# Kernel optimization log

Measured on AMD Instinct MI355X. Metric: run time of the kernel, lower is better.

## Reference

```python
import jax, jax.numpy as jnp
import numpy as np
import math

N = 10000; E = 160000; B = 16
H = 256; TD = 128; NB = 4; NL = 3; NAT = 100; CD = 3


def _silu(x):
    return x * jax.nn.sigmoid(x)


def _mlp2(x, w1, b1, w2, b2):
    return _silu(x @ w1 + b1) @ w2 + b2


def _ln(x, g, b):
    m = jnp.mean(x, -1, keepdims=True)
    v = jnp.mean((x - m) ** 2, -1, keepdims=True)
    return (x - m) / jnp.sqrt(v + 1e-5) * g + b


def _fwd(x_atoms, pos, edge_index, batch_idx, timesteps, conditions, emb,
         te_w1, te_b1, te_w2, te_b2, ce_w1, ce_b1, ce_w2, ce_b2,
         tp_w1, tp_b1, tp_w2, tp_b2, nm_w1, nm_b1, nm_w2, nm_b2,
         em_w1, em_b1, em_w2, em_b2, ln_g, ln_b,
         ao_w1, ao_b1, ao_w2, ao_b2, co_w1, co_b1, co_w2, co_b2):
    n = x_atoms.shape[0]
    row, col = edge_index[0], edge_index[1]  # row = source (x_j), col = target (x_i)
    h = emb[x_atoms]  # [N, H]
    half = TD // 2
    freqs = jnp.exp(jnp.arange(half, dtype=jnp.float32) * (-math.log(10000.0) / (half - 1)))
    ang = timesteps.astype(jnp.float32)[:, None] * freqs[None, :]
    time_emb = _mlp2(jnp.concatenate([jnp.sin(ang), jnp.cos(ang)], -1), te_w1, te_b1, te_w2, te_b2)
    time_emb = time_emb + _mlp2(conditions, ce_w1, ce_b1, ce_w2, ce_b2)  # [B, TD]
    rel = pos[row] - pos[col]
    dist = jnp.sqrt(jnp.sum(rel * rel, -1, keepdims=True))  # [E, 1]
    counts = jnp.maximum(
        jax.ops.segment_sum(jnp.ones((row.shape[0],), jnp.float32), col, num_segments=n), 1.0)[:, None]
    for b in range(NB):
        h = h + _mlp2(time_emb, tp_w1[b], tp_b1[b], tp_w2[b], tp_b2[b])[batch_idx]
        for l in range(NL):
            # message: edge_mlp(concat(x_i, x_j, dist)); PyG x_i = target = col, x_j = source = row
            msg = _mlp2(jnp.concatenate([h[col], h[row], dist], -1),
                        em_w1[b, l], em_b1[b, l], em_w2[b, l], em_b2[b, l])  # [E, H]
            agg = jax.ops.segment_sum(msg, col, num_segments=n) / counts  # mean aggregation
            h_new = _mlp2(h, nm_w1[b, l], nm_b1[b, l], nm_w2[b, l], nm_b2[b, l]) + agg
            h = _ln(h + h_new, ln_g[b, l], ln_b[b, l])
    atom = _mlp2(h, ao_w1, ao_b1, ao_w2, ao_b2)  # [N, NAT]
    coord = _mlp2(h, co_w1, co_b1, co_w2, co_b2)  # [N, 3]
    return atom, coord


def setup_inputs() -> dict:
    key = jax.random.key(0)
    ks = jax.random.split(key, 48)
    ki = iter(ks)

    def nrm(shape, s=0.02):
        return jax.random.normal(next(ki), shape, jnp.float32) * s

    x_atoms = jax.random.randint(next(ki), (N,), 0, NAT)
    pos = jax.random.normal(next(ki), (N, 3), jnp.float32)
    row = jax.random.randint(next(ki), (E,), 0, N)
    off = jax.random.randint(next(ki), (E,), 1, N)
    col = (row + off) % N  # avoid self-loops so dist > 0
    edge_index = jnp.stack([row, col])
    batch_idx = jnp.sort(jax.random.randint(next(ki), (N,), 0, B))
    timesteps = jax.random.randint(next(ki), (B,), 0, 1000)
    conditions = jax.random.normal(next(ki), (B, CD), jnp.float32)
    z = lambda s: jnp.zeros(s, jnp.float32)
    params = dict(
        emb=nrm((NAT, H)),
        te_w1=nrm((TD, 2 * TD)), te_b1=z((2 * TD,)), te_w2=nrm((2 * TD, TD)), te_b2=z((TD,)),
        ce_w1=nrm((CD, H)), ce_b1=z((H,)), ce_w2=nrm((H, TD)), ce_b2=z((TD,)),
        tp_w1=nrm((NB, TD, H)), tp_b1=z((NB, H)), tp_w2=nrm((NB, H, H)), tp_b2=z((NB, H)),
        nm_w1=nrm((NB, NL, H, H)), nm_b1=z((NB, NL, H)), nm_w2=nrm((NB, NL, H, H)), nm_b2=z((NB, NL, H)),
        em_w1=nrm((NB, NL, 2 * H + 1, H)), em_b1=z((NB, NL, H)), em_w2=nrm((NB, NL, H, H)), em_b2=z((NB, NL, H)),
        ln_g=jnp.ones((NB, NL, H), jnp.float32), ln_b=z((NB, NL, H)),
        ao_w1=nrm((H, H)), ao_b1=z((H,)), ao_w2=nrm((H, NAT)), ao_b2=z((NAT,)),
        co_w1=nrm((H, H)), co_b1=z((H,)), co_w2=nrm((H, 3)), co_b2=z((3,)),
    )
    return dict(x_atoms=x_atoms, pos=pos, edge_index=edge_index, batch_idx=batch_idx,
                timesteps=timesteps, conditions=conditions, **params)


def reference(x_atoms, pos, edge_index, batch_idx, timesteps, conditions, emb,
              te_w1, te_b1, te_w2, te_b2, ce_w1, ce_b1, ce_w2, ce_b2,
              tp_w1, tp_b1, tp_w2, tp_b2, nm_w1, nm_b1, nm_w2, nm_b2,
              em_w1, em_b1, em_w2, em_b2, ln_g, ln_b,
              ao_w1, ao_b1, ao_w2, ao_b2, co_w1, co_b1, co_w2, co_b2):
    return _fwd(x_atoms, pos, edge_index, batch_idx, timesteps, conditions, emb,
                te_w1, te_b1, te_w2, te_b2, ce_w1, ce_b1, ce_w2, ce_b2,
                tp_w1, tp_b1, tp_w2, tp_b2, nm_w1, nm_b1, nm_w2, nm_b2,
                em_w1, em_b1, em_w2, em_b2, ln_g, ln_b,
                ao_w1, ao_b1, ao_w2, ao_b2, co_w1, co_b1, co_w2, co_b2)
```

## Files before the change

### kernel.cpp

```cpp
#include <hip/hip_runtime.h>

typedef unsigned short u16;
typedef __attribute__((ext_vector_type(8))) short   bf16x8;
typedef __attribute__((ext_vector_type(4))) float   f32x4;
typedef __attribute__((ext_vector_type(4))) unsigned short u16x4;
typedef __attribute__((ext_vector_type(2))) unsigned short u16x2;

#define DEV __device__ __forceinline__

DEV float bf2f(u16 u){ return __uint_as_float(((unsigned)u)<<16); }
DEV u16 f2bf(float f){ unsigned x=__float_as_uint(f); unsigned r=x+0x7fffu+((x>>16)&1u); return (u16)(r>>16); }
DEV float silu_f(float x){
  float e = __expf(-x);
  return x * __builtin_amdgcn_rcpf(1.f + e);
}
DEV float ldf(const void* p, long i, int isbf){
  float r;
  if (isbf) r = bf2f(((const u16*)p)[i]);
  else      r = ((const float*)p)[i];
  return r;
}
template<int ISBF> DEV float LD(const void* p, long i){
  if (ISBF) return bf2f(((const u16*)p)[i]);
  return ((const float*)p)[i];
}
DEV int detect_bf(const void* lng){
  return (((const unsigned*)lng)[0] == 0x3F800000u) ? 0 : 1;
}

#define GLDS(g,l) __builtin_amdgcn_global_load_lds((const __attribute__((address_space(1))) void*)(g), (__attribute__((address_space(3))) void*)(l), 16, 0, 0)

DEV int xcd_swz(int bid, int nwg){
  int q = nwg >> 3, r = nwg & 7;
  int x = bid & 7, l = bid >> 3;
  return (x < r ? x*(q+1) : r*(q+1) + (x-r)*q) + l;
}

struct WTJob {
  const void* in; u16* out;
  int inoff, ims, obase, oms, istride, Ncin, ors, gx, gy;
};
struct WTJobs { WTJob j[8]; int tile0[8]; };

template<int ISBF>
DEV void wtall_body(const WTJobs& J, int bidx, float* tile ){
  int ji = 0;
  #pragma unroll
  for (int j=1;j<8;j++) if (bidx >= J.tile0[j]) ji = j;
  const WTJob& job = J.j[ji];
  int ti = bidx - J.tile0[ji];
  int kx = ti % job.gx;
  int jy = (ti / job.gx) % job.gy;
  long m  = ti / (job.gx * job.gy);
  int k0 = kx*64, j0 = jy*64;
  int t = threadIdx.x;
  int c = t & 63, r4 = t >> 6;
  #pragma unroll
  for (int pass=0; pass<16; pass++){
    int k = k0 + pass*4 + r4;
    int j = j0 + c;
    float v = 0.f;
    if (j < job.Ncin) v = LD<ISBF>(job.in, (long)job.inoff + m*job.ims + (long)k*job.istride + j);
    tile[(pass*4 + r4)*65 + c] = v;
  }
  __syncthreads();
  #pragma unroll
  for (int pass=0; pass<16; pass++){
    int j = j0 + pass*4 + r4;
    int k = k0 + c;
    job.out[m*job.oms + job.obase + (long)j*job.ors + k] = f2bf(tile[c*65 + pass*4 + r4]);
  }
}

DEV void pack_body(int pb, int isbf,
    const void* nm_b1, const void* em_b1, const void* nm_b2, const void* em_b2,
    const void* ln_g, const void* ln_b, const void* em_w1,
    const void* ao_b1, const void* co_b1, const void* ao_b2,
    const void* co_w2, const void* co_b2, float* pp){
  int i = pb*256 + threadIdx.x;
  if (i >= 22887) return;
  const int T1 = 3072;
  float v;
  if      (i < T1)    v = ldf(nm_b1, i, isbf);
  else if (i < 2*T1)  v = ldf(em_b1, i-T1, isbf);
  else if (i < 3*T1)  v = ldf(nm_b2, i-2*T1, isbf);
  else if (i < 4*T1)  v = ldf(em_b2, i-3*T1, isbf);
  else if (i < 5*T1)  v = ldf(ln_g, i-4*T1, isbf);
  else if (i < 6*T1)  v = ldf(ln_b, i-5*T1, isbf);
  else if (i < 7*T1){ int j=i-6*T1; int li=j>>8; v = ldf(em_w1, (long)li*513*256 + 512*256 + (j&255), isbf); }
  else if (i < 22016){ int j=i-21504; v = (j<256) ? ldf(ao_b1,j,isbf) : ldf(co_b1,j-256,isbf); }
  else if (i < 22116) v = ldf(ao_b2, i-22016, isbf);
  else if (i < 22884) v = ldf(co_w2, i-22116, isbf);
  else                v = ldf(co_b2, i-22884, isbf);
  pp[i] = v;
}

template<int ISBF>
DEV void edgegeo_body(int eb, const int* ei, const void* pos, float* dist, int* cnt, int E){
  int e = eb*256 + threadIdx.x;
  if (e >= E) return;
  int r = ei[e], c = ei[E + e];
  float dx = LD<ISBF>(pos,(long)r*3+0) - LD<ISBF>(pos,(long)c*3+0);
  float dy = LD<ISBF>(pos,(long)r*3+1) - LD<ISBF>(pos,(long)c*3+1);
  float dz = LD<ISBF>(pos,(long)r*3+2) - LD<ISBF>(pos,(long)c*3+2);
  dist[e] = sqrtf(dx*dx + dy*dy + dz*dz);
  atomicAdd(&cnt[c], 1);
}

DEV void time_body_f32(const int* tsteps, const float* cond,
    const float* te_w1,const float* te_b1,const float* te_w2,const float* te_b2,
    const float* ce_w1,const float* ce_b1,const float* ce_w2,const float* ce_b2,
    const float* tp_w1,const float* tp_b1,const float* tp_w2,const float* tp_b2,
    float* tpe, float* smem){
  float* wbuf = smem;
  float* sa = smem + 16384;
  float* sb = sa + 256;
  float* tm = sb + 256;
  float* tb = tm + 256;
  const int b4 = blockIdx.x >> 4, b = blockIdx.x & 15, t = threadIdx.x;
  const int wbase = (t >> 6) * 256;

  auto TISSUE = [&](const float* src, int buf){
    float* d = wbuf + buf*8192 + wbase;
    #pragma unroll
    for (int r=0;r<8;r++)
      GLDS(src + (long)r*1024 + t*4, d + r*1024);
  };

  float ts = (float)tsteps[b];
  if (t < 64){
    float coef = (float)(-9.210340371976184/63.0);
    float fr = __expf(coef * (float)t);
    float ang = ts * fr;
    sa[t] = sinf(ang); sa[64+t] = cosf(ang);
  }
  TISSUE(te_w1, 0);
  __syncthreads();
  float a1 = te_b1[t];
  for (int c=0;c<4;c++){
    if (c<3) TISSUE(te_w1 + (c+1)*8192, (c+1)&1);
    const float* wb = wbuf + (c&1)*8192;
    #pragma unroll 8
    for (int k=0;k<32;k++) a1 = fmaf(sa[c*32+k], wb[k*256+t], a1);
    __syncthreads();
  }
  sb[t] = silu_f(a1);
  TISSUE(te_w2, 0);
  __syncthreads();
  float te = (t<128) ? te_b2[t] : 0.f;
  for (int c=0;c<4;c++){
    if (c<3) TISSUE(te_w2 + (c+1)*8192, (c+1)&1);
    const float* wb = wbuf + (c&1)*8192;
    if (t < 128){
      #pragma unroll 8
      for (int k=0;k<64;k++) te = fmaf(sb[c*64+k], wb[k*128+t], te);
    }
    __syncthreads();
  }
  {
    float a2 = ce_b1[t];
    #pragma unroll
    for (int k=0;k<3;k++) a2 = fmaf(cond[b*3+k], ce_w1[k*256+t], a2);
    sa[t] = silu_f(a2);
  }
  TISSUE(ce_w2, 0);
  __syncthreads();
  float ce = (t<128) ? ce_b2[t] : 0.f;
  for (int c=0;c<4;c++){
    if (c<3) TISSUE(ce_w2 + (c+1)*8192, (c+1)&1);
    const float* wb = wbuf + (c&1)*8192;
    if (t < 128){
      #pragma unroll 8
      for (int k=0;k<64;k++) ce = fmaf(sa[c*64+k], wb[k*128+t], ce);
    }
    __syncthreads();
  }
  if (t < 128) tb[t] = te + ce;
  const float* W5 = tp_w1 + (long)b4*128*256;
  TISSUE(W5, 0);
  __syncthreads();
  float a3 = tp_b1[b4*256 + t];
  for (int c=0;c<4;c++){
    if (c<3) TISSUE(W5 + (c+1)*8192, (c+1)&1);
    const float* wb = wbuf + (c&1)*8192;
    #pragma unroll 8
    for (int k=0;k<32;k++) a3 = fmaf(tb[c*32+k], wb[k*256+t], a3);
    __syncthreads();
  }
  tm[t] = silu_f(a3);
  const float* W6 = tp_w2 + (long)b4*256*256;
  TISSUE(W6, 0);
  __syncthreads();
  float a4 = tp_b2[b4*256 + t];
  for (int c=0;c<8;c++){
    if (c<7) TISSUE(W6 + (c+1)*8192, (c+1)&1);
    const float* wb = wbuf + (c&1)*8192;
    #pragma unroll 8
    for (int k=0;k<32;k++) a4 = fmaf(tm[c*32+k], wb[k*256+t], a4);
    __syncthreads();
  }
  tpe[((long)b4*16 + b)*256 + t] = a4;
}

DEV void time_body_bf16(const int* tsteps, const u16* cond,
    const u16* te_w1,const u16* te_b1,const u16* te_w2,const u16* te_b2,
    const u16* ce_w1,const u16* ce_b1,const u16* ce_w2,const u16* ce_b2,
    const u16* tp_w1,const u16* tp_b1,const u16* tp_w2,const u16* tp_b2,
    float* tpe, float* smem){
  float* sa = smem; float* sb = smem+256; float* tm = smem+512; float* tb = smem+768;
  int b4 = blockIdx.x >> 4, b = blockIdx.x & 15, t = threadIdx.x;
  float ts = (float)tsteps[b];
  if (t < 64){
    float coef = (float)(-9.210340371976184/63.0);
    float fr = __expf(coef * (float)t);
    float ang = ts * fr;
    sa[t] = sinf(ang); sa[64+t] = cosf(ang);
  }
  __syncthreads();
  float a1 = bf2f(te_b1[t]);
  for (int k=0;k<128;k++) a1 += sa[k]*bf2f(te_w1[k*256+t]);
  __syncthreads();
  sb[t] = silu_f(a1);
  __syncthreads();
  float te = 0.f;
  if (t<128){
    te = bf2f(te_b2[t]);
    for (int k=0;k<256;k++) te += sb[k]*bf2f(te_w2[k*128+t]);
  }
  float a2 = bf2f(ce_b1[t]);
  for (int k=0;k<3;k++) a2 += bf2f(cond[b*3+k])*bf2f(ce_w1[k*256+t]);
  float t2v = silu_f(a2);
  __syncthreads();
  sa[t] = t2v;
  __syncthreads();
  if (t<128){
    float ce = bf2f(ce_b2[t]);
    for (int k=0;k<256;k++) ce += sa[k]*bf2f(ce_w2[k*128+t]);
    tb[t] = te + ce;
  }
  __syncthreads();
  float a3 = bf2f(tp_b1[b4*256+t]);
  for (int k=0;k<128;k++) a3 += tb[k]*bf2f(tp_w1[((long)b4*128+k)*256+t]);
  __syncthreads();
  tm[t] = silu_f(a3);
  __syncthreads();
  float a4 = bf2f(tp_b2[b4*256+t]);
  for (int k=0;k<256;k++) a4 += tm[k]*bf2f(tp_w2[((long)b4*256+k)*256+t]);
  tpe[((long)b4*16+b)*256+t] = a4;
}

__global__ __launch_bounds__(256) void k_startup(
    const int* tsteps, const void* cond,
    const void* te_w1,const void* te_b1,const void* te_w2,const void* te_b2,
    const void* ce_w1,const void* ce_b1,const void* ce_w2,const void* ce_b2,
    const void* tp_w1,const void* tp_b1,const void* tp_w2,const void* tp_b2,
    float* tpe,
    WTJobs J, int wt_n,
    const void* nm_b1,const void* em_b1,const void* nm_b2,const void* em_b2,
    const void* ln_g,const void* ln_b,const void* em_w1,
    const void* ao_b1,const void* co_b1,const void* ao_b2,const void* co_w2,const void* co_b2,
    float* pp, int pack_n,
    const int* ei, const void* pos, float* dist, int* cnt, int E)
{
  __shared__ __align__(16) float smem[17408];
  const int isbf = detect_bf(ln_g);
  int b = blockIdx.x;
  if (b < 64){
    if (isbf) time_body_bf16(tsteps, (const u16*)cond,
        (const u16*)te_w1,(const u16*)te_b1,(const u16*)te_w2,(const u16*)te_b2,
        (const u16*)ce_w1,(const u16*)ce_b1,(const u16*)ce_w2,(const u16*)ce_b2,
        (const u16*)tp_w1,(const u16*)tp_b1,(const u16*)tp_w2,(const u16*)tp_b2, tpe, smem);
    else time_body_f32(tsteps, (const float*)cond,
        (const float*)te_w1,(const float*)te_b1,(const float*)te_w2,(const float*)te_b2,
        (const float*)ce_w1,(const float*)ce_b1,(const float*)ce_w2,(const float*)ce_b2,
        (const float*)tp_w1,(const float*)tp_b1,(const float*)tp_w2,(const float*)tp_b2, tpe, smem);
  } else if (b < 64 + wt_n){
    if (isbf) wtall_body<1>(J, b-64, smem);
    else      wtall_body<0>(J, b-64, smem);
  } else if (b < 64 + wt_n + pack_n){
    pack_body(b - 64 - wt_n, isbf, nm_b1, em_b1, nm_b2, em_b2, ln_g, ln_b, em_w1,
              ao_b1, co_b1, ao_b2, co_w2, co_b2, pp);
  } else {
    int eb = b - 64 - wt_n - pack_n;
    if (isbf) edgegeo_body<1>(eb, ei, pos, dist, cnt, E);
    else      edgegeo_body<0>(eb, ei, pos, dist, cnt, E);
  }
}

__global__ __launch_bounds__(1024) void k_scan(const int* __restrict__ cnt, int* __restrict__ basep, int n){
  __shared__ int wsum[16];
  int t = threadIdx.x, w = t >> 6, lane = t & 63;
  int running = 0;
  int nch = (n + 1023) >> 10;
  for (int ch=0; ch<nch; ch++){
    int i = ch*1024 + t;
    int v = (i < n) ? cnt[i] : 0;
    int sc = v;
    #pragma unroll
    for (int off=1; off<64; off<<=1){
      int u = __shfl_up(sc, off, 64);
      if (lane >= off) sc += u;
    }
    if (lane == 63) wsum[w] = sc;
    __syncthreads();
    int wexcl = 0, tot = 0;
    #pragma unroll
    for (int j=0;j<16;j++){ int x = wsum[j]; if (j < w) wexcl += x; tot += x; }
    if (i < n) basep[i] = running + wexcl + sc - v;
    running += tot;
    __syncthreads();
  }
  if (t == 0) basep[n] = running;
}

__global__ __launch_bounds__(256) void k_scatter_embed(
    const int* __restrict__ ei, const int* __restrict__ basep,
    int* __restrict__ cursor, int* __restrict__ perm, int E,
    const int* __restrict__ xa, const void* __restrict__ emb, const void* __restrict__ lng,
    const float* __restrict__ tpe0, const int* __restrict__ bidx,
    float* __restrict__ h, u16* __restrict__ hb, int totalh){
  int b = blockIdx.x, t = threadIdx.x;
  int nsb = (E + 255) >> 8;
  if (b < nsb){
    int e = b*256 + t;
    if (e >= E) return;
    int c = ei[E + e];
    int p = atomicAdd(&cursor[c], 1);
    perm[basep[c] + p] = e;
  } else {
    int isbf = detect_bf(lng);
    int idx = (b - nsb)*256 + t;
    if (idx >= totalh) return;
    int row = idx >> 8, col = idx & 255;
    float v = ldf(emb, (long)xa[row]*256 + col, isbf) + tpe0[bidx[row]*256 + col];
    h[idx] = v;
    hb[idx] = f2bf(v);
  }
}

__global__ __launch_bounds__(256) void k_agg(
    const u16* __restrict__ PQ, const int* __restrict__ perm, const int* __restrict__ basep,
    const int* __restrict__ rows, const float* __restrict__ dist,
    const float* __restrict__ w1rf, const float* __restrict__ b1f,
    const int* __restrict__ cnt, u16* __restrict__ A2, int n){
  int w = threadIdx.x >> 6, lane = threadIdx.x & 63;
  int node = blockIdx.x*2 + (w >> 1);
  if (node >= n) return;
  int half = w & 1;
  int c0 = half*128 + lane*2;
  u16x2 pv = *(const u16x2*)&PQ[(long)node*512 + c0];
  float pb0 = bf2f(pv[0]) + b1f[c0];
  float pb1 = bf2f(pv[1]) + b1f[c0+1];
  float wr0 = w1rf[c0], wr1 = w1rf[c0+1];
  float acc0 = 0.f, acc1 = 0.f;
  int s = basep[node], e = basep[node+1];
  const u16* Qb = PQ + 256 + c0;
  for (int q0=s; q0<e; q0+=64){
    int m = e - q0; if (m > 64) m = 64;
    int   rl = 0; float dl = 0.f;
    if (lane < m){ int ed = perm[q0+lane]; rl = rows[ed]; dl = dist[ed]; }
    int q = 0;
    for (; q+8<=m; q+=8){
      u16x2 qv[8]; float dd[8];
      #pragma unroll
      for (int u=0;u<8;u++){
        int   r = __shfl(rl, q+u, 64);
        dd[u]   = __shfl(dl, q+u, 64);
        qv[u] = *(const u16x2*)&Qb[(long)r*512];
      }
      #pragma unroll
      for (int u=0;u<8;u++){
        acc0 += silu_f(fmaf(dd[u], wr0, pb0 + bf2f(qv[u][0])));
        acc1 += silu_f(fmaf(dd[u], wr1, pb1 + bf2f(qv[u][1])));
      }
    }
    if (q+4<=m){
      u16x2 qv[4]; float dd[4];
      #pragma unroll
      for (int u=0;u<4;u++){
        int   r = __shfl(rl, q+u, 64);
        dd[u]   = __shfl(dl, q+u, 64);
        qv[u] = *(const u16x2*)&Qb[(long)r*512];
      }
      #pragma unroll
      for (int u=0;u<4;u++){
        acc0 += silu_f(fmaf(dd[u], wr0, pb0 + bf2f(qv[u][0])));
        acc1 += silu_f(fmaf(dd[u], wr1, pb1 + bf2f(qv[u][1])));
      }
      q += 4;
    }
    for (; q<m; q++){
      int   r = __shfl(rl, q, 64);
      float d = __shfl(dl, q, 64);
      u16x2 qv = *(const u16x2*)&Qb[(long)r*512];
      acc0 += silu_f(fmaf(d, wr0, pb0 + bf2f(qv[0])));
      acc1 += silu_f(fmaf(d, wr1, pb1 + bf2f(qv[1])));
    }
  }
  int cc = cnt[node];
  float inv = __builtin_amdgcn_rcpf((float)(cc > 0 ? cc : 1));
  u16x2 o; o[0] = f2bf(acc0*inv); o[1] = f2bf(acc1*inv);
  *(u16x2*)&A2[(long)node*512 + 256 + c0] = o;
}

__global__ __launch_bounds__(256) void k_co2(
    const u16* __restrict__ UV, const float* __restrict__ w, const float* __restrict__ b,
    const void* __restrict__ lng, void* __restrict__ out, long n100, int n){
  int isbf = detect_bf(lng);
  int row = blockIdx.x*4 + (threadIdx.x >> 6);
  if (row >= n) return;
  int lane = threadIdx.x & 63;
  int k0 = lane*4;
  u16x4 vv = *(const u16x4*)&UV[(long)row*512 + 256 + k0];
  float a0=0.f, a1=0.f, a2=0.f;
  #pragma unroll
  for (int j=0;j<4;j++){
    float v = bf2f(vv[j]);
    a0 += v*w[(k0+j)*3+0];
    a1 += v*w[(k0+j)*3+1];
    a2 += v*w[(k0+j)*3+2];
  }
  #pragma unroll
  for (int o=32;o>=1;o>>=1){ a0 += __shfl_xor(a0,o,64); a1 += __shfl_xor(a1,o,64); a2 += __shfl_xor(a2,o,64); }
  if (lane == 0){
    float r0 = a0 + b[0], r1 = a1 + b[1], r2 = a2 + b[2];
    if (isbf){
      u16* o = (u16*)out + n100 + (long)row*3;
      o[0] = f2bf(r0); o[1] = f2bf(r1); o[2] = f2bf(r2);
    } else {
      float* o = (float*)out + n100 + (long)row*3;
      o[0] = r0; o[1] = r1; o[2] = r2;
    }
  }
}

template<int TM, int MODE>
__global__ __launch_bounds__(256) void k_gemm(
    const u16* __restrict__ A, int lda, const u16* __restrict__ Wt,
    void* __restrict__ D0, void* __restrict__ D1,
    const float* __restrict__ bf1,
    const void* __restrict__ lng, int M, int K, int nbn){
  constexpr int MR = TM/32;
  __shared__ __align__(16) u16 As[TM*64];
  __shared__ __align__(16) u16 Bs[128*64];
  const int bid = xcd_swz(blockIdx.x, gridDim.x);
  const int mb = bid / nbn, nb = bid - mb*nbn;
  const int bm0 = mb*TM, bn0 = nb*128;
  const int t = threadIdx.x;
  const int w = t >> 6, lane = t & 63;
  const int wr = w >> 1, wc = w & 1;
  const int swz8 = ((lane & 7) ^ (lane >> 3)) * 8;

  f32x4 acc[MR][4];
  #pragma unroll
  for (int m=0;m<MR;m++)
    #pragma unroll
    for (int n=0;n<4;n++){ f32x4 z = {0.f,0.f,0.f,0.f}; acc[m][n] = z; }

  long baseA[TM/32];
  #pragma unroll
  for (int i=0;i<TM/32;i++){
    int r = bm0 + i*32 + w*8 + (lane>>3);
    if (r > M-1) r = M-1;
    baseA[i] = (long)r*lda + swz8;
  }
  long baseB[4];
  #pragma unroll
  for (int i=0;i<4;i++){
    int r = bn0 + i*32 + w*8 + (lane>>3);
    baseB[i] = (long)r*K + swz8;
  }

  const int rA = lane & 15;
  const int sx = rA & 7;
  const int qhi = lane >> 4;

  for (int kt=0; kt<K; kt+=64){
    #pragma unroll
    for (int i=0;i<TM/32;i++) GLDS(A  + baseA[i] + kt, As + (i*32 + w*8)*64);
    #pragma unroll
    for (int i=0;i<4;i++)     GLDS(Wt + baseB[i] + kt, Bs + (i*32 + w*8)*64);
    __syncthreads();
    #pragma unroll
    for (int kk=0;kk<2;kk++){
      const int punit = ((kk*4 + qhi) ^ sx) * 8;
      bf16x8 af[MR], bv[4];
      #pragma unroll
      for (int m=0;m<MR;m++)
        af[m] = *(const bf16x8*)&As[(wr*(TM/2) + m*16 + rA)*64 + punit];
      #pragma unroll
      for (int n=0;n<4;n++)
        bv[n] = *(const bf16x8*)&Bs[(wc*64 + n*16 + rA)*64 + punit];
      #pragma unroll
      for (int m=0;m<MR;m++)
        #pragma unroll
        for (int n=0;n<4;n++)
          acc[m][n] = __builtin_amdgcn_mfma_f32_16x16x32_bf16(af[m], bv[n], acc[m][n], 0, 0, 0);
    }
    __syncthreads();
  }

  const int rg = lane >> 4, cix = lane & 15;
  const int isbf = (MODE==3) ? detect_bf(lng) : 0;
  #pragma unroll
  for (int n=0;n<4;n++){
    const int col = bn0 + wc*64 + n*16 + cix;
    float b1v = 0.f;
    if (MODE==0){ if (col>=512) b1v = bf1[col-512]; }
    else if (MODE==2){ b1v = bf1[col]; }
    else { if (col<100) b1v = bf1[col]; }
    #pragma unroll
    for (int m=0;m<MR;m++){
      const int rbase = bm0 + wr*(TM/2) + m*16 + rg*4;
      #pragma unroll
      for (int r=0;r<4;r++){
        const int row = rbase + r;
        if (row >= M) continue;
        float v = acc[m][n][r];
        if (MODE==0){
          if (col < 512) ((u16*)D0)[(long)row*512 + col] = f2bf(v);
          else           ((u16*)D1)[(long)row*512 + (col-512)] = f2bf(silu_f(v + b1v));
        } else if (MODE==2){
          ((u16*)D0)[(long)row*512 + col] = f2bf(silu_f(v + b1v));
        } else {
          if (col < 100){
            v += b1v;
            if (isbf) ((u16*)D0)[(long)row*100 + col] = f2bf(v);
            else      ((float*)D0)[(long)row*100 + col] = v;
          }
        }
      }
    }
  }
}

__global__ __launch_bounds__(256) void k_gemmln(
    const u16* __restrict__ A, const u16* __restrict__ Wt,
    float* __restrict__ h, u16* __restrict__ hb,
    const float* __restrict__ b1f, const float* __restrict__ b2f,
    const float* __restrict__ gf, const float* __restrict__ bbf,
    const int* __restrict__ cnt,
    const float* __restrict__ tpe, const int* __restrict__ bidx,
    int M, int K){
  __shared__ __align__(16) u16 As[32*64];
  __shared__ __align__(16) u16 Bs[256*64];
  const int bm0 = blockIdx.x*32;
  const int t = threadIdx.x;
  const int w = t >> 6, lane = t & 63;
  const int wc = w;
  const int swz8 = ((lane & 7) ^ (lane >> 3)) * 8;

  f32x4 acc[2][4];
  #pragma unroll
  for (int m=0;m<2;m++)
    #pragma unroll
    for (int n=0;n<4;n++){ f32x4 z = {0.f,0.f,0.f,0.f}; acc[m][n] = z; }

  long baseA;
  { int r = bm0 + w*8 + (lane>>3); if (r > M-1) r = M-1; baseA = (long)r*512 + swz8; }
  long baseB[8];
  #pragma unroll
  for (int i=0;i<8;i++){
    int r = i*32 + w*8 + (lane>>3);
    baseB[i] = (long)r*K + swz8;
  }

  const int rA = lane & 15;
  const int sx = rA & 7;
  const int qhi = lane >> 4;

  for (int kt=0; kt<K; kt+=64){
    GLDS(A + baseA + kt, As + (w*8)*64);
    #pragma unroll
    for (int i=0;i<8;i++) GLDS(Wt + baseB[i] + kt, Bs + (i*32 + w*8)*64);
    __syncthreads();
    #pragma unroll
    for (int kk=0;kk<2;kk++){
      const int punit = ((kk*4 + qhi) ^ sx) * 8;
      bf16x8 af[2], bv[4];
      #pragma unroll
      for (int m=0;m<2;m++)
        af[m] = *(const bf16x8*)&As[(m*16 + rA)*64 + punit];
      #pragma unroll
      for (int n=0;n<4;n++)
        bv[n] = *(const bf16x8*)&Bs[(wc*64 + n*16 + rA)*64 + punit];
      #pragma unroll
      for (int m=0;m<2;m++)
        #pragma unroll
        for (int n=0;n<4;n++)
          acc[m][n] = __builtin_amdgcn_mfma_f32_16x16x32_bf16(af[m], bv[n], acc[m][n], 0, 0, 0);
    }
    __syncthreads();
  }

  const int rg = lane >> 4, cix = lane & 15;
  float ps[2][4], pq[2][4];
  #pragma unroll
  for (int m=0;m<2;m++){
    #pragma unroll
    for (int r=0;r<4;r++){
      const int row = bm0 + m*16 + rg*4 + r;
      const int rowc = (row < M) ? row : (M-1);
      const float hmask = (cnt[rowc] > 0) ? 1.f : 0.f;
      float s = 0.f, q = 0.f;
      #pragma unroll
      for (int n=0;n<4;n++){
        const int col = wc*64 + n*16 + cix;
        float v = acc[m][n][r] + b1f[col] + hmask*b2f[col] + h[(long)rowc*256 + col];
        acc[m][n][r] = v;
        s += v; q += v*v;
      }
      ps[m][r] = s; pq[m][r] = q;
    }
  }
  #pragma unroll
  for (int m=0;m<2;m++)
    #pragma unroll
    for (int r=0;r<4;r++){
      #pragma unroll
      for (int o=8;o>=1;o>>=1){
        ps[m][r] += __shfl_xor(ps[m][r], o, 64);
        pq[m][r] += __shfl_xor(pq[m][r], o, 64);
      }
    }
  float* sred = (float*)As;
  if (cix == 0){
    #pragma unroll
    for (int m=0;m<2;m++)
      #pragma unroll
      for (int r=0;r<4;r++){
        int rl = m*16 + rg*4 + r;
        sred[w*32 + rl]       = ps[m][r];
        sred[128 + w*32 + rl] = pq[m][r];
      }
  }
  __syncthreads();
  #pragma unroll
  for (int m=0;m<2;m++){
    #pragma unroll
    for (int r=0;r<4;r++){
      const int rl = m*16 + rg*4 + r;
      const int row = bm0 + rl;
      if (row >= M) continue;
      float S = sred[rl] + sred[32+rl] + sred[64+rl] + sred[96+rl];
      float Q = sred[128+rl] + sred[160+rl] + sred[192+rl] + sred[224+rl];
      float mean = S * (1.f/256.f);
      float var  = Q * (1.f/256.f) - mean*mean;
      float rs = rsqrtf(var + 1e-5f);
      const float* tb = tpe ? (tpe + (long)bidx[row]*256) : nullptr;
      #pragma unroll
      for (int n=0;n<4;n++){
        const int col = wc*64 + n*16 + cix;
        float y = (acc[m][n][r]-mean)*rs*gf[col] + bbf[col];
        if (tb) y += tb[col];
        h[(long)row*256 + col] = y;
        hb[(long)row*256 + col] = f2bf(y);
      }
    }
  }
}

extern "C" void kernel_launch(void* const* d_in, const int* in_sizes, int n_in,
                              void* d_out, int out_size, void* d_ws, size_t ws_size,
                              hipStream_t stream)
{
  const int N  = in_sizes[0];
  const int E  = in_sizes[2] / 2;
  const int H  = 256;
  const int MB64  = (N + 63)/64;
  const int MB32  = (N + 31)/32;

  const int*  x_atoms = (const int*)d_in[0];
  const void* pos     = d_in[1];
  const int*  ei      = (const int*)d_in[2];
  const int*  bidx    = (const int*)d_in[3];
  const int*  tsteps  = (const int*)d_in[4];
  const void* cond    = d_in[5];
  const void* emb     = d_in[6];
  const void* te_w1   = d_in[7];
  const void* te_b1   = d_in[8];
  const void* te_w2   = d_in[9];
  const void* te_b2   = d_in[10];
  const void* ce_w1   = d_in[11];
  const void* ce_b1   = d_in[12];
  const void* ce_w2   = d_in[13];
  const void* ce_b2   = d_in[14];
  const void* tp_w1   = d_in[15];
  const void* tp_b1   = d_in[16];
  const void* tp_w2   = d_in[17];
  const void* tp_b2   = d_in[18];
  const void* nm_w1   = d_in[19];
  const void* nm_b1   = d_in[20];
  const void* nm_w2   = d_in[21];
  const void* nm_b2   = d_in[22];
  const void* em_w1   = d_in[23];
  const void* em_b1   = d_in[24];
  const void* em_w2   = d_in[25];
  const void* em_b2   = d_in[26];
  const void* ln_g    = d_in[27];
  const void* ln_b    = d_in[28];
  const void* ao_w1   = d_in[29];
  const void* ao_b1   = d_in[30];
  const void* ao_w2   = d_in[31];
  const void* ao_b2   = d_in[32];
  const void* co_w1   = d_in[33];
  const void* co_b1   = d_in[34];
  const void* co_w2   = d_in[35];
  const void* co_b2   = d_in[36];

  char* wp = (char*)d_ws;
  auto alloc = [&](size_t bytes)->char*{ char* p = wp; wp += (bytes + 255) & ~(size_t)255; return p; };
  float* h_f32   = (float*)alloc((size_t)N*H*4);
  u16*   hb16    = (u16*)  alloc((size_t)N*H*2);
  u16*   PQ      = (u16*)  alloc((size_t)N*512*2);
  u16*   A2      = (u16*)  alloc((size_t)N*512*2);
  u16*   UV      = PQ;
  float* dist    = (float*)alloc((size_t)E*4);
  int*   perm    = (int*)  alloc((size_t)E*4);
  int*   basep   = (int*)  alloc((size_t)(N+1)*4);
  size_t cntpad  = ((size_t)N*4 + 255) & ~(size_t)255;
  int*   cnt     = (int*)  alloc(2*cntpad);
  int*   cursor  = (int*)((char*)cnt + cntpad);
  float* tpe     = (float*)alloc((size_t)4*16*256*4);
  u16*   pqtW    = (u16*)  alloc((size_t)12*768*256*2);
  u16*   w2stk   = (u16*)  alloc((size_t)12*256*512*2);
  u16*   UVw     = (u16*)  alloc((size_t)512*256*2);
  u16*   ao_w2t  = (u16*)  alloc((size_t)128*256*2);
  float* pp      = (float*)alloc((size_t)22887*4);

  const float* nm_b1f = pp;
  const float* em_b1f = pp + 3072;
  const float* nm_b2f = pp + 6144;
  const float* em_b2f = pp + 9216;
  const float* ln_gf  = pp + 12288;
  const float* ln_bf  = pp + 15360;
  const float* w1rf   = pp + 18432;
  const float* headbf = pp + 21504;
  const float* ao_b2f = pp + 22016;
  const float* co_w2f = pp + 22116;
  const float* co_b2f = pp + 22884;

  hipMemsetAsync(cnt, 0, 2*cntpad, stream);

  WTJobs J;
  int tacc = 0;
  auto setjob = [&](int idx, const void* in, int inoff, int ims, int istride, int Ncin,
                    u16* out, int obase, int ors, int oms, int gx, int gy, int gz){
    J.j[idx] = WTJob{ in, out, inoff, ims, obase, oms, istride, Ncin, ors, gx, gy };
    J.tile0[idx] = tacc;
    tacc += gx*gy*gz;
  };
  setjob(0, em_w1, 0,        513*256, 256, 256, pqtW,  0,        256, 768*256, 4, 4, 12);
  setjob(1, em_w1, 256*256,  513*256, 256, 256, pqtW,  256*256,  256, 768*256, 4, 4, 12);
  setjob(2, nm_w1, 0,        256*256, 256, 256, pqtW,  512*256,  256, 768*256, 4, 4, 12);
  setjob(3, nm_w2, 0,        256*256, 256, 256, w2stk, 0,        512, 256*512, 4, 4, 12);
  setjob(4, em_w2, 0,        256*256, 256, 256, w2stk, 256,      512, 256*512, 4, 4, 12);
  setjob(5, ao_w1, 0,        0,       256, 256, UVw,   0,        256, 0,       4, 4, 1);
  setjob(6, co_w1, 0,        0,       256, 256, UVw,   256*256,  256, 0,       4, 4, 1);
  setjob(7, ao_w2, 0,        0,       100, 100, ao_w2t,0,        256, 0,       4, 2, 1);
  const int wt_n = tacc;
  const int pack_n = (22887 + 255)/256;
  const int eg_n = (E + 255)/256;
  k_startup<<<64 + wt_n + pack_n + eg_n, 256, 0, stream>>>(
      tsteps, cond, te_w1, te_b1, te_w2, te_b2, ce_w1, ce_b1, ce_w2, ce_b2,
      tp_w1, tp_b1, tp_w2, tp_b2, tpe,
      J, wt_n,
      nm_b1, em_b1, nm_b2, em_b2, ln_g, ln_b, em_w1,
      ao_b1, co_b1, ao_b2, co_w2, co_b2, pp, pack_n,
      ei, pos, dist, cnt, E);

  k_scan<<<1, 1024, 0, stream>>>(cnt, basep, N);

  k_scatter_embed<<<eg_n + (N*H + 255)/256, 256, 0, stream>>>(
      ei, basep, cursor, perm, E,
      x_atoms, emb, ln_g, tpe, bidx, h_f32, hb16, N*H);

  for (int b4 = 0; b4 < 4; b4++){
    for (int l = 0; l < 3; l++){
      int li = b4*3 + l;
      k_gemm<64,0><<<MB64*6, 256, 0, stream>>>(hb16, 256, pqtW + (long)li*768*256,
                                               PQ, A2, nm_b1f + li*256,
                                               ln_g, N, 256, 6);
      k_agg<<<(N+1)/2, 256, 0, stream>>>(PQ, perm, basep, ei, dist,
                                         w1rf + li*256, em_b1f + li*256, cnt, A2, N);
      const float* tpe_next = (l == 2 && b4 < 3) ? (tpe + (long)(b4+1)*16*256) : nullptr;
      k_gemmln<<<MB32, 256, 0, stream>>>(A2, w2stk + (long)li*256*512,
                                         h_f32, hb16,
                                         nm_b2f + li*256, em_b2f + li*256,
                                         ln_gf + li*256, ln_bf + li*256,
                                         cnt, tpe_next, bidx, N, 512);
    }
  }

  k_gemm<64,2><<<MB64*4, 256, 0, stream>>>(hb16, 256, UVw, UV, nullptr, headbf,
                                           ln_g, N, 256, 4);
  k_gemm<64,3><<<MB64*1, 256, 0, stream>>>(UV, 512, ao_w2t, d_out, nullptr, ao_b2f,
                                           ln_g, N, 256, 1);
  k_co2<<<(N+3)/4, 256, 0, stream>>>(UV, co_w2f, co_b2f, ln_g, d_out, (long)N*100, N);
}
```

Baseline: 742.1 us.

## Move node-MLP first GEMM into aggregation kernel and shrink startup LDS

The per-layer projection GEMM now computes only the P/Q edge projections. The node-MLP first-layer GEMM (silu output written into A2) moves into the aggregation launch as extra blocks, so that GEMM work runs alongside the memory-bound gather aggregation in a single kernel. Separately, the startup time-embedding path uses half-size double-buffered weight chunks, cutting the startup kernel's shared memory from about 68KB to 36KB so more blocks can be resident. The cost is more chunk iterations and barriers in the time MLP, plus mixed block types sharing one launch's resource footprint.

```diff
diff --git a/kernel.cpp b/kernel.cpp
--- a/kernel.cpp
+++ b/kernel.cpp
@@ -113,7 +113,7 @@
     const float* tp_w1,const float* tp_b1,const float* tp_w2,const float* tp_b2,
     float* tpe, float* smem){
   float* wbuf = smem;
-  float* sa = smem + 16384;
+  float* sa = smem + 8192;
   float* sb = sa + 256;
   float* tm = sb + 256;
   float* tb = tm + 256;
@@ -121,9 +121,9 @@
   const int wbase = (t >> 6) * 256;
 
   auto TISSUE = [&](const float* src, int buf){
-    float* d = wbuf + buf*8192 + wbase;
-    #pragma unroll
-    for (int r=0;r<8;r++)
+    float* d = wbuf + buf*4096 + wbase;
+    #pragma unroll
+    for (int r=0;r<4;r++)
       GLDS(src + (long)r*1024 + t*4, d + r*1024);
   };
 
@@ -137,23 +137,23 @@
   TISSUE(te_w1, 0);
   __syncthreads();
   float a1 = te_b1[t];
-  for (int c=0;c<4;c++){
-    if (c<3) TISSUE(te_w1 + (c+1)*8192, (c+1)&1);
-    const float* wb = wbuf + (c&1)*8192;
-    #pragma unroll 8
-    for (int k=0;k<32;k++) a1 = fmaf(sa[c*32+k], wb[k*256+t], a1);
+  for (int c=0;c<8;c++){
+    if (c<7) TISSUE(te_w1 + (c+1)*4096, (c+1)&1);
+    const float* wb = wbuf + (c&1)*4096;
+    #pragma unroll
+    for (int k=0;k<16;k++) a1 = fmaf(sa[c*16+k], wb[k*256+t], a1);
     __syncthreads();
   }
   sb[t] = silu_f(a1);
   TISSUE(te_w2, 0);
   __syncthreads();
   float te = (t<128) ? te_b2[t] : 0.f;
-  for (int c=0;c<4;c++){
-    if (c<3) TISSUE(te_w2 + (c+1)*8192, (c+1)&1);
-    const float* wb = wbuf + (c&1)*8192;
+  for (int c=0;c<8;c++){
+    if (c<7) TISSUE(te_w2 + (c+1)*4096, (c+1)&1);
+    const float* wb = wbuf + (c&1)*4096;
     if (t < 128){
-      #pragma unroll 8
-      for (int k=0;k<64;k++) te = fmaf(sb[c*64+k], wb[k*128+t], te);
+      #pragma unroll
+      for (int k=0;k<32;k++) te = fmaf(sb[c*32+k], wb[k*128+t], te);
     }
     __syncthreads();
   }
@@ -166,12 +166,12 @@
   TISSUE(ce_w2, 0);
   __syncthreads();
   float ce = (t<128) ? ce_b2[t] : 0.f;
-  for (int c=0;c<4;c++){
-    if (c<3) TISSUE(ce_w2 + (c+1)*8192, (c+1)&1);
-    const float* wb = wbuf + (c&1)*8192;
+  for (int c=0;c<8;c++){
+    if (c<7) TISSUE(ce_w2 + (c+1)*4096, (c+1)&1);
+    const float* wb = wbuf + (c&1)*4096;
     if (t < 128){
-      #pragma unroll 8
-      for (int k=0;k<64;k++) ce = fmaf(sa[c*64+k], wb[k*128+t], ce);
+      #pragma unroll
+      for (int k=0;k<32;k++) ce = fmaf(sa[c*32+k], wb[k*128+t], ce);
     }
     __syncthreads();
   }
@@ -180,11 +180,11 @@
   TISSUE(W5, 0);
   __syncthreads();
   float a3 = tp_b1[b4*256 + t];
-  for (int c=0;c<4;c++){
-    if (c<3) TISSUE(W5 + (c+1)*8192, (c+1)&1);
-    const float* wb = wbuf + (c&1)*8192;
-    #pragma unroll 8
-    for (int k=0;k<32;k++) a3 = fmaf(tb[c*32+k], wb[k*256+t], a3);
+  for (int c=0;c<8;c++){
+    if (c<7) TISSUE(W5 + (c+1)*4096, (c+1)&1);
+    const float* wb = wbuf + (c&1)*4096;
+    #pragma unroll
+    for (int k=0;k<16;k++) a3 = fmaf(tb[c*16+k], wb[k*256+t], a3);
     __syncthreads();
   }
   tm[t] = silu_f(a3);
@@ -192,11 +192,11 @@
   TISSUE(W6, 0);
   __syncthreads();
   float a4 = tp_b2[b4*256 + t];
-  for (int c=0;c<8;c++){
-    if (c<7) TISSUE(W6 + (c+1)*8192, (c+1)&1);
-    const float* wb = wbuf + (c&1)*8192;
-    #pragma unroll 8
-    for (int k=0;k<32;k++) a4 = fmaf(tm[c*32+k], wb[k*256+t], a4);
+  for (int c=0;c<16;c++){
+    if (c<15) TISSUE(W6 + (c+1)*4096, (c+1)&1);
+    const float* wb = wbuf + (c&1)*4096;
+    #pragma unroll
+    for (int k=0;k<16;k++) a4 = fmaf(tm[c*16+k], wb[k*256+t], a4);
     __syncthreads();
   }
   tpe[((long)b4*16 + b)*256 + t] = a4;
@@ -262,7 +262,7 @@
     float* pp, int pack_n,
     const int* ei, const void* pos, float* dist, int* cnt, int E)
 {
-  __shared__ __align__(16) float smem[17408];
+  __shared__ __align__(16) float smem[9088];
   const int isbf = detect_bf(ln_g);
   int b = blockIdx.x;
   if (b < 64){
@@ -338,69 +338,152 @@
   }
 }
 
-__global__ __launch_bounds__(256) void k_agg(
+__global__ __launch_bounds__(256) void k_tagg(
+    const u16* __restrict__ hb, const u16* __restrict__ WtT,
+    u16* __restrict__ A2, const float* __restrict__ nmb1f,
     const u16* __restrict__ PQ, const int* __restrict__ perm, const int* __restrict__ basep,
     const int* __restrict__ rows, const float* __restrict__ dist,
     const float* __restrict__ w1rf, const float* __restrict__ b1f,
-    const int* __restrict__ cnt, u16* __restrict__ A2, int n){
-  int w = threadIdx.x >> 6, lane = threadIdx.x & 63;
-  int node = blockIdx.x*2 + (w >> 1);
-  if (node >= n) return;
-  int half = w & 1;
-  int c0 = half*128 + lane*2;
-  u16x2 pv = *(const u16x2*)&PQ[(long)node*512 + c0];
-  float pb0 = bf2f(pv[0]) + b1f[c0];
-  float pb1 = bf2f(pv[1]) + b1f[c0+1];
-  float wr0 = w1rf[c0], wr1 = w1rf[c0+1];
-  float acc0 = 0.f, acc1 = 0.f;
-  int s = basep[node], e = basep[node+1];
-  const u16* Qb = PQ + 256 + c0;
-  for (int q0=s; q0<e; q0+=64){
-    int m = e - q0; if (m > 64) m = 64;
-    int   rl = 0; float dl = 0.f;
-    if (lane < m){ int ed = perm[q0+lane]; rl = rows[ed]; dl = dist[ed]; }
-    int q = 0;
-    for (; q+8<=m; q+=8){
-      u16x2 qv[8]; float dd[8];
-      #pragma unroll
-      for (int u=0;u<8;u++){
-        int   r = __shfl(rl, q+u, 64);
-        dd[u]   = __shfl(dl, q+u, 64);
-        qv[u] = *(const u16x2*)&Qb[(long)r*512];
+    const int* __restrict__ cnt, int M, int nT)
+{
+  __shared__ __align__(16) u16 As[64*64];
+  __shared__ __align__(16) u16 Bs[128*64];
+
+  if (blockIdx.x >= nT){
+    int w = threadIdx.x >> 6, lane = threadIdx.x & 63;
+    int node = (blockIdx.x - nT)*2 + (w >> 1);
+    if (node >= M) return;
+    int half = w & 1;
+    int c0 = half*128 + lane*2;
+    u16x2 pv = *(const u16x2*)&PQ[(long)node*512 + c0];
+    float pb0 = bf2f(pv[0]) + b1f[c0];
+    float pb1 = bf2f(pv[1]) + b1f[c0+1];
+    float wr0 = w1rf[c0], wr1 = w1rf[c0+1];
+    float acc0 = 0.f, acc1 = 0.f;
+    int s = basep[node], e = basep[node+1];
+    const u16* Qb = PQ + 256 + c0;
+    for (int q0=s; q0<e; q0+=64){
+      int m = e - q0; if (m > 64) m = 64;
+      int   rl = 0; float dl = 0.f;
+      if (lane < m){ int ed = perm[q0+lane]; rl = rows[ed]; dl = dist[ed]; }
+      int q = 0;
+      for (; q+8<=m; q+=8){
+        u16x2 qv[8]; float dd[8];
+        #pragma unroll
+        for (int u=0;u<8;u++){
+          int   r = __shfl(rl, q+u, 64);
+          dd[u]   = __shfl(dl, q+u, 64);
+          qv[u] = *(const u16x2*)&Qb[(long)r*512];
+        }
+        #pragma unroll
+        for (int u=0;u<8;u++){
+          acc0 += silu_f(fmaf(dd[u], wr0, pb0 + bf2f(qv[u][0])));
+          acc1 += silu_f(fmaf(dd[u], wr1, pb1 + bf2f(qv[u][1])));
+        }
       }
-      #pragma unroll
-      for (int u=0;u<8;u++){
-        acc0 += silu_f(fmaf(dd[u], wr0, pb0 + bf2f(qv[u][0])));
-        acc1 += silu_f(fmaf(dd[u], wr1, pb1 + bf2f(qv[u][1])));
+      if (q+4<=m){
+        u16x2 qv[4]; float dd[4];
+        #pragma unroll
+        for (int u=0;u<4;u++){
+          int   r = __shfl(rl, q+u, 64);
+          dd[u]   = __shfl(dl, q+u, 64);
+          qv[u] = *(const u16x2*)&Qb[(long)r*512];
+        }
+        #pragma unroll
+        for (int u=0;u<4;u++){
+          acc0 += silu_f(fmaf(dd[u], wr0, pb0 + bf2f(qv[u][0])));
+          acc1 += silu_f(fmaf(dd[u], wr1, pb1 + bf2f(qv[u][1])));
+        }
+        q += 4;
       }
-    }
-    if (q+4<=m){
-      u16x2 qv[4]; float dd[4];
-      #pragma unroll
-      for (int u=0;u<4;u++){
-        int   r = __shfl(rl, q+u, 64);
-        dd[u]   = __shfl(dl, q+u, 64);
-        qv[u] = *(const u16x2*)&Qb[(long)r*512];
+      for (; q<m; q++){
+        int   r = __shfl(rl, q, 64);
+        float d = __shfl(dl, q, 64);
+        u16x2 qv = *(const u16x2*)&Qb[(long)r*512];
+        acc0 += silu_f(fmaf(d, wr0, pb0 + bf2f(qv[0])));
+        acc1 += silu_f(fmaf(d, wr1, pb1 + bf2f(qv[1])));
       }
-      #pragma unroll
-      for (int u=0;u<4;u++){
-        acc0 += silu_f(fmaf(dd[u], wr0, pb0 + bf2f(qv[u][0])));
-        acc1 += silu_f(fmaf(dd[u], wr1, pb1 + bf2f(qv[u][1])));
+    }
+    int cc = cnt[node];
+    float inv = __builtin_amdgcn_rcpf((float)(cc > 0 ? cc : 1));
+    u16x2 o; o[0] = f2bf(acc0*inv); o[1] = f2bf(acc1*inv);
+    *(u16x2*)&A2[(long)node*512 + 256 + c0] = o;
+    return;
+  }
+
+  const int bid = blockIdx.x;
+  const int mb = bid >> 1, nb = bid & 1;
+  const int bm0 = mb*64, bn0 = nb*128;
+  const int t = threadIdx.x;
+  const int w = t >> 6, lane = t & 63;
+  const int wr = w >> 1, wc = w & 1;
+  const int swz8 = ((lane & 7) ^ (lane >> 3)) * 8;
+
+  f32x4 acc[2][4];
+  #pragma unroll
+  for (int m=0;m<2;m++)
+    #pragma unroll
+    for (int n=0;n<4;n++){ f32x4 z = {0.f,0.f,0.f,0.f}; acc[m][n] = z; }
+
+  long baseA[2];
+  #pragma unroll
+  for (int i=0;i<2;i++){
+    int r = bm0 + i*32 + w*8 + (lane>>3);
+    if (r > M-1) r = M-1;
+    baseA[i] = (long)r*256 + swz8;
+  }
+  long baseB[4];
+  #pragma unroll
+  for (int i=0;i<4;i++){
+    int r = bn0 + i*32 + w*8 + (lane>>3);
+    baseB[i] = (long)r*256 + swz8;
+  }
+
+  const int rA = lane & 15;
+  const int sx = rA & 7;
+  const int qhi = lane >> 4;
+
+  for (int kt=0; kt<256; kt+=64){
+    #pragma unroll
+    for (int i=0;i<2;i++) GLDS(hb  + baseA[i] + kt, As + (i*32 + w*8)*64);
+    #pragma unroll
+    for (int i=0;i<4;i++) GLDS(WtT + baseB[i] + kt, Bs + (i*32 + w*8)*64);
+    __syncthreads();
+    #pragma unroll
+    for (int kk=0;kk<2;kk++){
+      const int punit = ((kk*4 + qhi) ^ sx) * 8;
+      bf16x8 af[2], bv[4];
+      #pragma unroll
+      for (int m=0;m<2;m++)
+        af[m] = *(const bf16x8*)&As[(wr*32 + m*16 + rA)*64 + punit];
+      #pragma unroll
+      for (int n=0;n<4;n++)
+        bv[n] = *(const bf16x8*)&Bs[(wc*64 + n*16 + rA)*64 + punit];
+      #pragma unroll
+      for (int m=0;m<2;m++)
+        #pragma unroll
+        for (int n=0;n<4;n++)
+          acc[m][n] = __builtin_amdgcn_mfma_f32_16x16x32_bf16(af[m], bv[n], acc[m][n], 0, 0, 0);
+    }
+    __syncthreads();
+  }
+
+  const int rg = lane >> 4, cix = lane & 15;
+  #pragma unroll
+  for (int n=0;n<4;n++){
+    const int col = bn0 + wc*64 + n*16 + cix;
+    float b1v = nmb1f[col];
+    #pragma unroll
+    for (int m=0;m<2;m++){
+      const int rbase = bm0 + wr*32 + m*16 + rg*4;
+      #pragma unroll
+      for (int r=0;r<4;r++){
+        const int row = rbase + r;
+        if (row >= M) continue;
+        A2[(long)row*512 + col] = f2bf(silu_f(acc[m][n][r] + b1v));
       }
-      q += 4;
-    }
-    for (; q<m; q++){
-      int   r = __shfl(rl, q, 64);
-      float d = __shfl(dl, q, 64);
-      u16x2 qv = *(const u16x2*)&Qb[(long)r*512];
-      acc0 += silu_f(fmaf(d, wr0, pb0 + bf2f(qv[0])));
-      acc1 += silu_f(fmaf(d, wr1, pb1 + bf2f(qv[1])));
-    }
-  }
-  int cc = cnt[node];
-  float inv = __builtin_amdgcn_rcpf((float)(cc > 0 ? cc : 1));
-  u16x2 o; o[0] = f2bf(acc0*inv); o[1] = f2bf(acc1*inv);
-  *(u16x2*)&A2[(long)node*512 + 256 + c0] = o;
+    }
+  }
 }
 
 __global__ __launch_bounds__(256) void k_co2(
@@ -437,7 +520,7 @@
 template<int TM, int MODE>
 __global__ __launch_bounds__(256) void k_gemm(
     const u16* __restrict__ A, int lda, const u16* __restrict__ Wt,
-    void* __restrict__ D0, void* __restrict__ D1,
+    void* __restrict__ D0,
     const float* __restrict__ bf1,
     const void* __restrict__ lng, int M, int K, int nbn){
   constexpr int MR = TM/32;
@@ -506,9 +589,8 @@
   for (int n=0;n<4;n++){
     const int col = bn0 + wc*64 + n*16 + cix;
     float b1v = 0.f;
-    if (MODE==0){ if (col>=512) b1v = bf1[col-512]; }
-    else if (MODE==2){ b1v = bf1[col]; }
-    else { if (col<100) b1v = bf1[col]; }
+    if (MODE==2){ b1v = bf1[col]; }
+    else if (MODE==3){ if (col<100) b1v = bf1[col]; }
     #pragma unroll
     for (int m=0;m<MR;m++){
       const int rbase = bm0 + wr*(TM/2) + m*16 + rg*4;
@@ -518,8 +600,7 @@
         if (row >= M) continue;
         float v = acc[m][n][r];
         if (MODE==0){
-          if (col < 512) ((u16*)D0)[(long)row*512 + col] = f2bf(v);
-          else           ((u16*)D1)[(long)row*512 + (col-512)] = f2bf(silu_f(v + b1v));
+          ((u16*)D0)[(long)row*512 + col] = f2bf(v);
         } else if (MODE==2){
           ((u16*)D0)[(long)row*512 + col] = f2bf(silu_f(v + b1v));
         } else {
@@ -775,14 +856,16 @@
       ei, basep, cursor, perm, E,
       x_atoms, emb, ln_g, tpe, bidx, h_f32, hb16, N*H);
 
+  const int nT = MB64*2;
   for (int b4 = 0; b4 < 4; b4++){
     for (int l = 0; l < 3; l++){
       int li = b4*3 + l;
-      k_gemm<64,0><<<MB64*6, 256, 0, stream>>>(hb16, 256, pqtW + (long)li*768*256,
-                                               PQ, A2, nm_b1f + li*256,
-                                               ln_g, N, 256, 6);
-      k_agg<<<(N+1)/2, 256, 0, stream>>>(PQ, perm, basep, ei, dist,
-                                         w1rf + li*256, em_b1f + li*256, cnt, A2, N);
+      k_gemm<64,0><<<MB64*4, 256, 0, stream>>>(hb16, 256, pqtW + (long)li*768*256,
+                                               PQ, nullptr, ln_g, N, 256, 4);
+      k_tagg<<<nT + (N+1)/2, 256, 0, stream>>>(hb16, pqtW + (long)li*768*256 + 512*256,
+                                               A2, nm_b1f + li*256,
+                                               PQ, perm, basep, ei, dist,
+                                               w1rf + li*256, em_b1f + li*256, cnt, N, nT);
       const float* tpe_next = (l == 2 && b4 < 3) ? (tpe + (long)(b4+1)*16*256) : nullptr;
       k_gemmln<<<MB32, 256, 0, stream>>>(A2, w2stk + (long)li*256*512,
                                          h_f32, hb16,
@@ -792,9 +875,9 @@
     }
   }
 
-  k_gemm<64,2><<<MB64*4, 256, 0, stream>>>(hb16, 256, UVw, UV, nullptr, headbf,
+  k_gemm<64,2><<<MB64*4, 256, 0, stream>>>(hb16, 256, UVw, UV, headbf,
                                            ln_g, N, 256, 4);
-  k_gemm<64,3><<<MB64*1, 256, 0, stream>>>(UV, 512, ao_w2t, d_out, nullptr, ao_b2f,
+  k_gemm<64,3><<<MB64*1, 256, 0, stream>>>(UV, 512, ao_w2t, d_out, ao_b2f,
                                            ln_g, N, 256, 1);
   k_co2<<<(N+3)/4, 256, 0, stream>>>(UV, co_w2f, co_b2f, ln_g, d_out, (long)N*100, N);
 }
```

Result: slower. 787.5 us (+6.1%).
